# Kernel tuning notes

Measured on AMD Instinct MI355X. Metric: run time of the kernel, lower is better.

## Reference

```python
import jax, jax.numpy as jnp
import numpy as np

P_DROP = 0.2
NEG_SLOPE = 0.2


def setup_inputs() -> dict:
    key = jax.random.key(0)
    ks = jax.random.split(key, 12)
    N, E = 50000, 800000
    IN, H1, H2, OUT = 256, 256, 128, 64
    x = jax.random.normal(ks[0], (N, IN), dtype=jnp.float32)
    adj_rows = jax.random.randint(ks[1], (E,), 0, N, dtype=jnp.int32)
    adj_cols = jax.random.randint(ks[2], (E,), 0, N, dtype=jnp.int32)
    adj_vals = jax.random.uniform(ks[3], (E,), dtype=jnp.float32)
    W1 = jax.random.normal(ks[4], (H1, IN), dtype=jnp.float32) * (1.0 / np.sqrt(IN))
    b1 = jax.random.normal(ks[5], (H1,), dtype=jnp.float32) * 0.01
    W2 = jax.random.normal(ks[6], (H2, H1), dtype=jnp.float32) * (1.0 / np.sqrt(H1))
    b2 = jax.random.normal(ks[7], (H2,), dtype=jnp.float32) * 0.01
    W3 = jax.random.normal(ks[8], (OUT, H2), dtype=jnp.float32) * (1.0 / np.sqrt(H2))
    b3 = jax.random.normal(ks[9], (OUT,), dtype=jnp.float32) * 0.01
    mask1 = jax.random.bernoulli(ks[10], 1.0 - P_DROP, (N, H1))
    mask2 = jax.random.bernoulli(ks[11], 1.0 - P_DROP, (N, H2))
    return {"x": x, "adj_rows": adj_rows, "adj_cols": adj_cols, "adj_vals": adj_vals,
            "W1": W1, "b1": b1, "W2": W2, "b2": b2, "W3": W3, "b3": b3,
            "mask1": mask1, "mask2": mask2}


def _spmm(rows, cols, vals, h, n_nodes):
    # sparse adjacency matmul: out[r] = sum_e vals[e] * h[cols[e]] for rows[e]==r
    msgs = vals[:, None] * h[cols]  # [E, d] irregular gather
    return jax.ops.segment_sum(msgs, rows, num_segments=n_nodes)


def _gcn_layer(x, W, b, rows, cols, vals, n_nodes):
    h = x @ W.T + b  # nn.Linear
    return _spmm(rows, cols, vals, h, n_nodes)


def reference(x, adj_rows, adj_cols, adj_vals, W1, b1, W2, b2, W3, b3, mask1, mask2):
    N = x.shape[0]
    keep = 1.0 / (1.0 - P_DROP)
    h = _gcn_layer(x, W1, b1, adj_rows, adj_cols, adj_vals, N)
    h = jnp.where(h >= 0, h, NEG_SLOPE * h)
    h = jnp.where(mask1, h * keep, 0.0)
    h = _gcn_layer(h, W2, b2, adj_rows, adj_cols, adj_vals, N)
    h = jnp.where(h >= 0, h, NEG_SLOPE * h)
    h = jnp.where(mask2, h * keep, 0.0)
    z = _gcn_layer(h, W3, b3, adj_rows, adj_cols, adj_vals, N)
    return z
```

## Files before the change

### kernel.cpp

```cpp
#include <hip/hip_runtime.h>


typedef unsigned short ushort_t;
typedef __attribute__((ext_vector_type(8))) short bf16x8;
typedef __attribute__((ext_vector_type(4))) float f32x4;
typedef __attribute__((ext_vector_type(2))) unsigned int u32x2;
typedef __attribute__((ext_vector_type(4))) unsigned int u32x4;

__device__ __forceinline__ float bf2f(ushort_t u) {
  return __uint_as_float(((unsigned int)u) << 16);
}
__device__ __forceinline__ ushort_t f2bf(float f) {
  unsigned int u = __float_as_uint(f);
  return (ushort_t)((u + 0x7FFFu + ((u >> 16) & 1u)) >> 16);
}
__device__ __forceinline__ float read_f(const void* p, int fm, size_t i) {
  return fm ? bf2f(((const ushort_t*)p)[i]) : ((const float*)p)[i];
}

__device__ __forceinline__ size_t frag_off(int m, int k, int K) {
  return (size_t)(m >> 4) * 16 * K + ((size_t)(k >> 5) << 9) +
         (((k >> 3) & 3) << 7) + ((m & 15) << 3) + (k & 7);
}

__device__ __forceinline__ bool mask_keep(const void* mask, int mm, size_t o) {
  switch (mm) {
    case 1:  return ((const int*)mask)[o] != 0;
    case 2:  return ((const unsigned int*)mask)[o] != 0u;
    case 3:  return ((const ushort_t*)mask)[o] != 0;
    default: return ((const unsigned char*)mask)[o] != 0;
  }
}

__global__ void prep_kernel(const void* __restrict__ x,
                            const void* __restrict__ m1,
                            const void* __restrict__ m2,
                            int* __restrict__ modes,
                            int* __restrict__ zero_region, int zn) {
  if (blockIdx.x == 0) {
    __shared__ int bfok;
    if (threadIdx.x == 0) bfok = 1;
    __syncthreads();
    for (int i = threadIdx.x; i < 8192; i += blockDim.x) {
      ushort_t h = ((const ushort_t*)x)[i];
      int e = (h >> 7) & 0xFF;
      if (!(h == 0 || (e >= 95 && e <= 133))) atomicAnd(&bfok, 0);
    }
    __syncthreads();
    if (threadIdx.x == 0) modes[0] = bfok;
  } else if (blockIdx.x <= 2) {
    const void* p = (blockIdx.x == 1) ? m1 : m2;
    __shared__ int ok[4];
    if (threadIdx.x < 4) ok[threadIdx.x] = 1;
    __syncthreads();
    for (int i = threadIdx.x; i < 4096; i += blockDim.x) {
      unsigned int w = ((const unsigned int*)p)[i];
      if (!(w == 0u || w == 1u)) atomicAnd(&ok[0], 0);
      if (!(w == 0u || w == 0x3F800000u)) atomicAnd(&ok[1], 0);
      unsigned int h16 = w >> 16, l16 = w & 0xFFFFu;
      if (!((h16 == 0u || h16 == 0x3F80u) && (l16 == 0u || l16 == 0x3F80u)))
        atomicAnd(&ok[2], 0);
      if (((w | (w >> 8) | (w >> 16) | (w >> 24)) & 0xFEu) != 0u) atomicAnd(&ok[3], 0);
    }
    __syncthreads();
    if (threadIdx.x == 0)
      modes[blockIdx.x] = ok[0] ? 1 : (ok[1] ? 2 : (ok[2] ? 3 : 0));
  } else {
    int i = (blockIdx.x - 3) * blockDim.x + threadIdx.x;
    int stride = (gridDim.x - 3) * blockDim.x;
    for (; i < zn; i += stride) zero_region[i] = 0;
  }
}

__global__ void hist_kernel(const int* __restrict__ rows, int* __restrict__ cnt, int E) {
  int i = blockIdx.x * blockDim.x + threadIdx.x;
  int stride = gridDim.x * blockDim.x;
  for (; i < E; i += stride) atomicAdd(&cnt[rows[i]], 1);
}

__global__ void scan_part_kernel(const int* __restrict__ cnt, int* __restrict__ part, int n) {
  __shared__ int s[256];
  int i = blockIdx.x * 256 + threadIdx.x;
  s[threadIdx.x] = (i < n) ? cnt[i] : 0;
  __syncthreads();
  for (int off = 128; off > 0; off >>= 1) {
    if (threadIdx.x < off) s[threadIdx.x] += s[threadIdx.x + off];
    __syncthreads();
  }
  if (threadIdx.x == 0) part[blockIdx.x] = s[0];
}

__global__ __launch_bounds__(1024) void scan_top_kernel(int* __restrict__ part, int P) {
  __shared__ int s[1024];
  int t = threadIdx.x;
  int v = (t < P) ? part[t] : 0;
  s[t] = v;
  __syncthreads();
  for (int off = 1; off < 1024; off <<= 1) {
    int x = s[t];
    int y = (t >= off) ? s[t - off] : 0;
    __syncthreads();
    s[t] = x + y;
    __syncthreads();
  }
  if (t < P) part[t] = s[t] - v;
}

__global__ void scan_apply_kernel(const int* __restrict__ cnt, const int* __restrict__ part,
                                  int* __restrict__ row_start, int n) {
  __shared__ int s[256];
  int base = part[blockIdx.x];
  int i = blockIdx.x * 256 + threadIdx.x;
  int v = (i < n) ? cnt[i] : 0;
  s[threadIdx.x] = v;
  __syncthreads();
  for (int off = 1; off < 256; off <<= 1) {
    int x = s[threadIdx.x];
    int y = (threadIdx.x >= off) ? s[threadIdx.x - off] : 0;
    __syncthreads();
    s[threadIdx.x] = x + y;
    __syncthreads();
  }
  if (i < n) row_start[i] = base + s[threadIdx.x] - v;
  if (i == n - 1) row_start[n] = base + s[threadIdx.x];
}

__global__ void scatter_convert_kernel(
    const int* __restrict__ rows, const int* __restrict__ cols,
    const void* __restrict__ vals, const int* __restrict__ fm_p,
    const int* __restrict__ row_start, int* __restrict__ fill,
    int2* __restrict__ ecv, int E,
    const void* __restrict__ W1, const void* __restrict__ W2, const void* __restrict__ W3,
    const void* __restrict__ b1, const void* __restrict__ b2, const void* __restrict__ b3,
    const void* __restrict__ x,
    ushort_t* __restrict__ whi, ushort_t* __restrict__ wlo,
    float* __restrict__ biasf, ushort_t* __restrict__ xbf,
    int n1, int n2, int n3, int h1, int h2, int h3, int K1, int K2, int K3, int nx) {
  int fm = *fm_p;
  if (blockIdx.x < 1024) {
    int i = blockIdx.x * blockDim.x + threadIdx.x;
    int stride = 1024 * blockDim.x;
    for (; i < E; i += stride) {
      int r = rows[i];
      int pos = atomicAdd(&fill[r], 1);
      int idx = row_start[r] + pos;
      ecv[idx] = make_int2(cols[i], __float_as_int(read_f(vals, fm, i)));
    }
  } else {
    int wtot = n1 + n2 + n3;
    int btot = h1 + h2 + h3;
    int nx4 = nx / 4;
    int total = wtot + btot + nx4;
    int i = (blockIdx.x - 1024) * blockDim.x + threadIdx.x;
    int stride = (gridDim.x - 1024) * blockDim.x;
    for (; i < total; i += stride) {
      if (i < wtot) {
        const void* src; int j, K; size_t base;
        if (i < n1) { src = W1; j = i; K = K1; base = 0; }
        else if (i < n1 + n2) { src = W2; j = i - n1; K = K2; base = n1; }
        else { src = W3; j = i - n1 - n2; K = K3; base = (size_t)n1 + n2; }
        int n = j / K, k = j - n * K;
        float v = read_f(src, fm, j);
        ushort_t h = f2bf(v);
        size_t o = base + frag_off(n, k, K);
        whi[o] = h;
        wlo[o] = f2bf(v - bf2f(h));
      } else if (i < wtot + btot) {
        int k = i - wtot;
        const void* src; int j;
        if (k < h1) { src = b1; j = k; }
        else if (k < h1 + h2) { src = b2; j = k - h1; }
        else { src = b3; j = k - h1 - h2; }
        biasf[k] = read_f(src, fm, j);
      } else {
        int k4 = i - wtot - btot;
        int m = k4 / (K1 / 4);
        int k0 = (k4 - m * (K1 / 4)) * 4;
        ushort_t p0, p1, p2, p3;
        if (fm == 0) {
          f32x4 v = ((const f32x4*)x)[k4];
          p0 = f2bf(v[0]); p1 = f2bf(v[1]); p2 = f2bf(v[2]); p3 = f2bf(v[3]);
        } else {
          const ushort_t* xb = (const ushort_t*)x + (size_t)k4 * 4;
          p0 = xb[0]; p1 = xb[1]; p2 = xb[2]; p3 = xb[3];
        }
        size_t o = frag_off(m, k0, K1);
        *(u32x2*)(xbf + o) = (u32x2){
            (unsigned int)p0 | ((unsigned int)p1 << 16),
            (unsigned int)p2 | ((unsigned int)p3 << 16)};
      }
    }
  }
}

template<int KC>
__global__ __launch_bounds__(256) void gemm_breg_kernel(
    const ushort_t* __restrict__ A,
    const ushort_t* __restrict__ Whi, const ushort_t* __restrict__ Wlo,
    const float* __restrict__ bias, ushort_t* __restrict__ g, int ldg,
    int M, int nct) {
  const int K = KC * 32;
  int wave = threadIdx.x >> 6, lane = threadIdx.x & 63;
  int gw = blockIdx.x * 4 + wave;
  int NW = gridDim.x * 4;
  int mr = lane & 15, quad = lane >> 4;
  int ct = gw % nct;
  int nrt = (M + 15) >> 4;
  int ntasks = nct * nrt;
  if (gw >= ntasks) return;

  bf16x8 wh[KC], wl[KC];
  {
    const ushort_t* wp = Whi + (size_t)ct * 16 * K + lane * 8;
    const ushort_t* wq = Wlo + (size_t)ct * 16 * K + lane * 8;
#pragma unroll
    for (int kc = 0; kc < KC; ++kc) {
      wh[kc] = *(const bf16x8*)(wp + kc * 512);
      wl[kc] = *(const bf16x8*)(wq + kc * 512);
    }
  }
  int col = ct * 16 + mr;
  float bv = bias[col];

  int task = gw;
  bf16x8 af[KC];
  {
    const ushort_t* ap = A + (size_t)(task / nct) * 16 * K + lane * 8;
#pragma unroll
    for (int kc = 0; kc < KC; ++kc) af[kc] = *(const bf16x8*)(ap + kc * 512);
  }

#pragma unroll 1
  for (;;) {
    int next = task + NW;
    bool has_next = next < ntasks;
    bf16x8 afn[KC];
    if (has_next) {
      const ushort_t* ap = A + (size_t)(next / nct) * 16 * K + lane * 8;
#pragma unroll
      for (int kc = 0; kc < KC; ++kc) afn[kc] = *(const bf16x8*)(ap + kc * 512);
    }

    f32x4 acc[4];
#pragma unroll
    for (int t = 0; t < 4; ++t) acc[t] = (f32x4){0.f, 0.f, 0.f, 0.f};
#pragma unroll
    for (int kc = 0; kc < KC; ++kc) {
      acc[(2 * kc) & 3] = __builtin_amdgcn_mfma_f32_16x16x32_bf16(af[kc], wh[kc], acc[(2 * kc) & 3], 0, 0, 0);
      acc[(2 * kc + 1) & 3] = __builtin_amdgcn_mfma_f32_16x16x32_bf16(af[kc], wl[kc], acc[(2 * kc + 1) & 3], 0, 0, 0);
    }
    int m0 = (task / nct) * 16;
#pragma unroll
    for (int r = 0; r < 4; ++r) {
      int row = m0 + quad * 4 + r;
      float s = ((acc[0][r] + acc[1][r]) + (acc[2][r] + acc[3][r])) + bv;
      if (row < M) g[(size_t)row * ldg + col] = f2bf(s);
    }
    if (!has_next) break;
#pragma unroll
    for (int kc = 0; kc < KC; ++kc) af[kc] = afn[kc];
    task = next;
  }
}

template<int MODE, int VEC>
__global__ __launch_bounds__(256) void spmm8_kernel(
    const int* __restrict__ row_start, const int2* __restrict__ ecv,
    const ushort_t* __restrict__ G, int D,
    const void* __restrict__ mask, const int* __restrict__ mmode_p,
    void* __restrict__ outp, int N) {
  __shared__ ushort_t stage[1024];
  int wave = threadIdx.x >> 6, lane = threadIdx.x & 63;
  int r = blockIdx.x * 4 + wave;
  bool active = r < N;
  float a[VEC];
#pragma unroll
  for (int q = 0; q < VEC; ++q) a[q] = 0.f;
  int f0 = lane * VEC;

  if (active) {
    int e  = __builtin_amdgcn_readfirstlane(row_start[r]);
    int e1 = __builtin_amdgcn_readfirstlane(row_start[r + 1]);
    for (; e + 8 <= e1; e += 8) {
      int2 cv[8];
#pragma unroll
      for (int j = 0; j < 8; ++j) cv[j] = ecv[e + j];
      if (VEC == 4) {
        u32x2 gg[8];
#pragma unroll
        for (int j = 0; j < 8; ++j)
          gg[j] = *(const u32x2*)(G + (size_t)cv[j].x * D + f0);
#pragma unroll
        for (int j = 0; j < 8; ++j) {
          float v = __int_as_float(cv[j].y);
          a[0] += v * bf2f((ushort_t)gg[j][0]);
          a[1] += v * bf2f((ushort_t)(gg[j][0] >> 16));
          a[2] += v * bf2f((ushort_t)gg[j][1]);
          a[3] += v * bf2f((ushort_t)(gg[j][1] >> 16));
        }
      } else if (VEC == 2) {
        unsigned int gg[8];
#pragma unroll
        for (int j = 0; j < 8; ++j)
          gg[j] = *(const unsigned int*)(G + (size_t)cv[j].x * D + f0);
#pragma unroll
        for (int j = 0; j < 8; ++j) {
          float v = __int_as_float(cv[j].y);
          a[0] += v * bf2f((ushort_t)gg[j]);
          a[1] += v * bf2f((ushort_t)(gg[j] >> 16));
        }
      } else {
        ushort_t h[8];
#pragma unroll
        for (int j = 0; j < 8; ++j) h[j] = G[(size_t)cv[j].x * D + f0];
#pragma unroll
        for (int j = 0; j < 8; ++j) a[0] += __int_as_float(cv[j].y) * bf2f(h[j]);
      }
    }
    if (e < e1) {
      int idx[8]; float v[8];
#pragma unroll
      for (int j = 0; j < 8; ++j) {
        int ee = e + j;
        bool ok = ee < e1;
        int2 cv = ecv[ok ? ee : e1 - 1];
        idx[j] = cv.x;
        v[j] = ok ? __int_as_float(cv.y) : 0.f;
      }
      if (VEC == 4) {
        u32x2 gg[8];
#pragma unroll
        for (int j = 0; j < 8; ++j)
          gg[j] = *(const u32x2*)(G + (size_t)idx[j] * D + f0);
#pragma unroll
        for (int j = 0; j < 8; ++j) {
          a[0] += v[j] * bf2f((ushort_t)gg[j][0]);
          a[1] += v[j] * bf2f((ushort_t)(gg[j][0] >> 16));
          a[2] += v[j] * bf2f((ushort_t)gg[j][1]);
          a[3] += v[j] * bf2f((ushort_t)(gg[j][1] >> 16));
        }
      } else if (VEC == 2) {
        unsigned int gg[8];
#pragma unroll
        for (int j = 0; j < 8; ++j)
          gg[j] = *(const unsigned int*)(G + (size_t)idx[j] * D + f0);
#pragma unroll
        for (int j = 0; j < 8; ++j) {
          a[0] += v[j] * bf2f((ushort_t)gg[j]);
          a[1] += v[j] * bf2f((ushort_t)(gg[j] >> 16));
        }
      } else {
        ushort_t h[8];
#pragma unroll
        for (int j = 0; j < 8; ++j) h[j] = G[(size_t)idx[j] * D + f0];
#pragma unroll
        for (int j = 0; j < 8; ++j) a[0] += v[j] * bf2f(h[j]);
      }
    }
  }

  if (MODE == 1) {
    if (active) {
      size_t om = (size_t)r * D + f0;
      int mm = *mmode_p;
      bool keep[VEC];
      if (mm == 1 || mm == 2) {
        if (VEC == 4) {
          u32x4 mv = *(const u32x4*)((const unsigned int*)mask + om);
#pragma unroll
          for (int q = 0; q < VEC; ++q) keep[q] = mv[q] != 0u;
        } else if (VEC == 2) {
          u32x2 mv = *(const u32x2*)((const unsigned int*)mask + om);
#pragma unroll
          for (int q = 0; q < VEC; ++q) keep[q] = mv[q] != 0u;
        } else {
          keep[0] = ((const unsigned int*)mask)[om] != 0u;
        }
      } else {
#pragma unroll
        for (int q = 0; q < VEC; ++q) keep[q] = mask_keep(mask, mm, om + q);
      }
#pragma unroll
      for (int q = 0; q < VEC; ++q) {
        float t = a[q];
        t = (t >= 0.f) ? t : 0.2f * t;
        t = keep[q] ? t * 1.25f : 0.f;
        stage[wave * D + f0 + q] = f2bf(t);
      }
    }
    __syncthreads();
    if (threadIdx.x < D) {
      int g = threadIdx.x >> 3, s = threadIdx.x & 7;
      int kc = g >> 2, quad = g & 3;
      int sr = s >> 1;
      int r0 = blockIdx.x * 4;
      if (r0 + sr < N) {
        int kk = kc * 32 + quad * 8 + (s & 1) * 4;
        size_t dst = (size_t)(r0 >> 4) * 16 * D + ((size_t)kc << 9) +
                     (quad << 7) + ((r0 & 15) << 3) + s * 4;
        *(u32x2*)((ushort_t*)outp + dst) = *(const u32x2*)(stage + sr * D + kk);
      }
    }
  } else {
    if (active) {
      size_t o = (size_t)r * D + f0;
#pragma unroll
      for (int q = 0; q < VEC; ++q) ((float*)outp)[o + q] = a[q];
    }
  }
}

extern "C" void kernel_launch(void* const* d_in, const int* in_sizes, int n_in,
                              void* d_out, int out_size, void* d_ws, size_t ws_size,
                              hipStream_t stream) {
  const void* x     = d_in[0];
  const int*  rows  = (const int*)d_in[1];
  const int*  cols  = (const int*)d_in[2];
  const void* vals  = d_in[3];
  const void* W1    = d_in[4];
  const void* b1    = d_in[5];
  const void* W2    = d_in[6];
  const void* b2    = d_in[7];
  const void* W3    = d_in[8];
  const void* b3    = d_in[9];
  const void* mask1 = d_in[10];
  const void* mask2 = d_in[11];

  const int H1  = in_sizes[5];
  const int H2  = in_sizes[7];
  const int OUT = in_sizes[9];
  const int IN  = in_sizes[4] / H1;
  const int N   = in_sizes[0] / IN;
  const int E   = in_sizes[1];
  const int W1n = in_sizes[4], W2n = in_sizes[6], W3n = in_sizes[8];
  const int Np  = ((N + 15) / 16) * 16;

  char* ws = (char*)d_ws;
  size_t off = 0;
  auto alloc = [&](size_t bytes) -> void* {
    void* p = ws + off;
    off = (off + bytes + 255) & ~(size_t)255;
    return p;
  };
  int*      modes     = (int*)alloc(4 * 4);
  int*      row_start = (int*)alloc((size_t)(N + 1) * 4);
  int*      cnt       = (int*)alloc((size_t)N * 8);
  int*      part      = (int*)alloc(1024 * 4);
  int2*     ecv       = (int2*)alloc((size_t)E * 8);
  ushort_t* whi       = (ushort_t*)alloc((size_t)(W1n + W2n + W3n) * 2);
  ushort_t* wlo       = (ushort_t*)alloc((size_t)(W1n + W2n + W3n) * 2);
  float*    biasf     = (float*)alloc((size_t)(H1 + H2 + OUT) * 4);
  ushort_t* bufA      = (ushort_t*)alloc((size_t)Np * H1 * 2);
  ushort_t* bufB      = (ushort_t*)alloc((size_t)Np * H1 * 2);
  ushort_t* bufC      = (ushort_t*)alloc((size_t)Np * H1 * 2);

  int* fmode = modes;
  int* mm1   = modes + 1;
  int* mm2   = modes + 2;
  int* fill  = cnt + N;
  ushort_t* w1hi = whi,             *w1lo = wlo;
  ushort_t* w2hi = whi + W1n,       *w2lo = wlo + W1n;
  ushort_t* w3hi = whi + W1n + W2n, *w3lo = wlo + W1n + W2n;

  prep_kernel<<<259, 256, 0, stream>>>(x, mask1, mask2, modes, cnt, 2 * N);

  const int P = (N + 255) / 256;
  hist_kernel<<<1024, 256, 0, stream>>>(rows, cnt, E);
  scan_part_kernel<<<P, 256, 0, stream>>>(cnt, part, N);
  scan_top_kernel<<<1, 1024, 0, stream>>>(part, P);
  scan_apply_kernel<<<P, 256, 0, stream>>>(cnt, part, row_start, N);

  scatter_convert_kernel<<<3072, 256, 0, stream>>>(
      rows, cols, vals, fmode, row_start, fill, ecv, E,
      W1, W2, W3, b1, b2, b3, x, whi, wlo, biasf, bufA,
      W1n, W2n, W3n, H1, H2, OUT, IN, H1, H2, N * IN);

  const int GEMM_BLOCKS = 1024;
  int spmm_grid = (N + 3) / 4;

  gemm_breg_kernel<8><<<GEMM_BLOCKS, 256, 0, stream>>>(
      bufA, w1hi, w1lo, biasf, bufB, H1, N, H1 / 16);
  spmm8_kernel<1, 4><<<spmm_grid, 256, 0, stream>>>(
      row_start, ecv, bufB, H1, mask1, mm1, bufC, N);
  gemm_breg_kernel<8><<<GEMM_BLOCKS, 256, 0, stream>>>(
      bufC, w2hi, w2lo, biasf + H1, bufB, H2, N, H2 / 16);
  spmm8_kernel<1, 2><<<spmm_grid, 256, 0, stream>>>(
      row_start, ecv, bufB, H2, mask2, mm2, bufA, N);
  gemm_breg_kernel<4><<<GEMM_BLOCKS, 256, 0, stream>>>(
      bufA, w3hi, w3lo, biasf + H1 + H2, bufB, OUT, N, OUT / 16);
  spmm8_kernel<0, 1><<<spmm_grid, 256, 0, stream>>>(
      row_start, ecv, bufB, OUT, nullptr, fmode, d_out, N);
}
```

Baseline: 438.3 us.

## Partition edge scatter by row range and read bf16 x directly in GEMM

The edge scatter now splits blocks into eight row-range partitions. Each block scans a stripe of edges and only handles edges whose destination row falls in its partition, which is meant to improve locality of the atomic fill counters and ecv writes. The cost is that every partition reads the full rows array, so rows is read eight times. When the input is bf16 (fm==1), the x re-layout pass is skipped and the first GEMM loads A fragments straight from row-major x. The mask reading also gains vectorized paths for 16-bit and byte masks.

Measured after the change: 432.1 us. Within noise of the previous version (-1.4%).

```diff
diff --git a/kernel.cpp b/kernel.cpp
--- a/kernel.cpp
+++ b/kernel.cpp
@@ -135,13 +135,20 @@
     const void* __restrict__ x,
     ushort_t* __restrict__ whi, ushort_t* __restrict__ wlo,
     float* __restrict__ biasf, ushort_t* __restrict__ xbf,
-    int n1, int n2, int n3, int h1, int h2, int h3, int K1, int K2, int K3, int nx) {
+    int n1, int n2, int n3, int h1, int h2, int h3, int K1, int K2, int K3,
+    int nx, int Nrows) {
   int fm = *fm_p;
   if (blockIdx.x < 1024) {
-    int i = blockIdx.x * blockDim.x + threadIdx.x;
-    int stride = 1024 * blockDim.x;
+    int part = blockIdx.x & 7;
+    int stripe = blockIdx.x >> 3;
+    float pscale = 8.0f / (float)Nrows;
+    int i = stripe * blockDim.x + threadIdx.x;
+    int stride = 128 * blockDim.x;
     for (; i < E; i += stride) {
       int r = rows[i];
+      int p = (int)((float)r * pscale);
+      p = (p > 7) ? 7 : p;
+      if (p != part) continue;
       int pos = atomicAdd(&fill[r], 1);
       int idx = row_start[r] + pos;
       ecv[idx] = make_int2(cols[i], __float_as_int(read_f(vals, fm, i)));
@@ -149,7 +156,7 @@
   } else {
     int wtot = n1 + n2 + n3;
     int btot = h1 + h2 + h3;
-    int nx4 = nx / 4;
+    int nx4 = (fm == 1) ? 0 : nx / 4;
     int total = wtot + btot + nx4;
     int i = (blockIdx.x - 1024) * blockDim.x + threadIdx.x;
     int stride = (gridDim.x - 1024) * blockDim.x;
@@ -176,14 +183,8 @@
         int k4 = i - wtot - btot;
         int m = k4 / (K1 / 4);
         int k0 = (k4 - m * (K1 / 4)) * 4;
-        ushort_t p0, p1, p2, p3;
-        if (fm == 0) {
-          f32x4 v = ((const f32x4*)x)[k4];
-          p0 = f2bf(v[0]); p1 = f2bf(v[1]); p2 = f2bf(v[2]); p3 = f2bf(v[3]);
-        } else {
-          const ushort_t* xb = (const ushort_t*)x + (size_t)k4 * 4;
-          p0 = xb[0]; p1 = xb[1]; p2 = xb[2]; p3 = xb[3];
-        }
+        f32x4 v = ((const f32x4*)x)[k4];
+        ushort_t p0 = f2bf(v[0]), p1 = f2bf(v[1]), p2 = f2bf(v[2]), p3 = f2bf(v[3]);
         size_t o = frag_off(m, k0, K1);
         *(u32x2*)(xbf + o) = (u32x2){
             (unsigned int)p0 | ((unsigned int)p1 << 16),
@@ -194,8 +195,28 @@
 }
 
 template<int KC>
+__device__ __forceinline__ void load_afrag(const ushort_t* __restrict__ A,
+                                           const ushort_t* __restrict__ Xrow,
+                                           bool rowA, int mtile, int K,
+                                           int lane, int mr, int quad, int M,
+                                           bf16x8* dst) {
+  if (rowA) {
+    int rr = mtile * 16 + mr;
+    if (rr >= M) rr = M - 1;
+    const ushort_t* ap = Xrow + (size_t)rr * K + quad * 8;
+#pragma unroll
+    for (int kc = 0; kc < KC; ++kc) dst[kc] = *(const bf16x8*)(ap + kc * 32);
+  } else {
+    const ushort_t* ap = A + (size_t)mtile * 16 * K + lane * 8;
+#pragma unroll
+    for (int kc = 0; kc < KC; ++kc) dst[kc] = *(const bf16x8*)(ap + kc * 512);
+  }
+}
+
+template<int KC>
 __global__ __launch_bounds__(256) void gemm_breg_kernel(
     const ushort_t* __restrict__ A,
+    const ushort_t* __restrict__ Xrow, const int* __restrict__ fm_p,
     const ushort_t* __restrict__ Whi, const ushort_t* __restrict__ Wlo,
     const float* __restrict__ bias, ushort_t* __restrict__ g, int ldg,
     int M, int nct) {
@@ -209,6 +230,8 @@
   int ntasks = nct * nrt;
   if (gw >= ntasks) return;
 
+  bool rowA = (Xrow != nullptr) && (*fm_p != 0);
+
   bf16x8 wh[KC], wl[KC];
   {
     const ushort_t* wp = Whi + (size_t)ct * 16 * K + lane * 8;
@@ -224,22 +247,15 @@
 
   int task = gw;
   bf16x8 af[KC];
-  {
-    const ushort_t* ap = A + (size_t)(task / nct) * 16 * K + lane * 8;
-#pragma unroll
-    for (int kc = 0; kc < KC; ++kc) af[kc] = *(const bf16x8*)(ap + kc * 512);
-  }
+  load_afrag<KC>(A, Xrow, rowA, task / nct, K, lane, mr, quad, M, af);
 
 #pragma unroll 1
   for (;;) {
     int next = task + NW;
     bool has_next = next < ntasks;
     bf16x8 afn[KC];
-    if (has_next) {
-      const ushort_t* ap = A + (size_t)(next / nct) * 16 * K + lane * 8;
-#pragma unroll
-      for (int kc = 0; kc < KC; ++kc) afn[kc] = *(const bf16x8*)(ap + kc * 512);
-    }
+    if (has_next)
+      load_afrag<KC>(A, Xrow, rowA, next / nct, K, lane, mr, quad, M, afn);
 
     f32x4 acc[4];
 #pragma unroll
@@ -376,9 +392,28 @@
         } else {
           keep[0] = ((const unsigned int*)mask)[om] != 0u;
         }
+      } else if (mm == 3) {
+        if (VEC == 4) {
+          u32x2 mv = *(const u32x2*)((const ushort_t*)mask + om);
+          keep[0] = (mv[0] & 0xFFFFu) != 0u; keep[1] = (mv[0] >> 16) != 0u;
+          keep[2] = (mv[1] & 0xFFFFu) != 0u; keep[3] = (mv[1] >> 16) != 0u;
+        } else if (VEC == 2) {
+          unsigned int mv = *(const unsigned int*)((const ushort_t*)mask + om);
+          keep[0] = (mv & 0xFFFFu) != 0u; keep[1] = (mv >> 16) != 0u;
+        } else {
+          keep[0] = ((const ushort_t*)mask)[om] != 0;
+        }
       } else {
-#pragma unroll
-        for (int q = 0; q < VEC; ++q) keep[q] = mask_keep(mask, mm, om + q);
+        if (VEC == 4) {
+          unsigned int mv = *(const unsigned int*)((const unsigned char*)mask + om);
+          keep[0] = (mv & 0xFFu) != 0u;        keep[1] = ((mv >> 8) & 0xFFu) != 0u;
+          keep[2] = ((mv >> 16) & 0xFFu) != 0u; keep[3] = (mv >> 24) != 0u;
+        } else if (VEC == 2) {
+          unsigned int mv = *(const unsigned short*)((const unsigned char*)mask + om);
+          keep[0] = (mv & 0xFFu) != 0u; keep[1] = ((mv >> 8) & 0xFFu) != 0u;
+        } else {
+          keep[0] = ((const unsigned char*)mask)[om] != 0;
+        }
       }
 #pragma unroll
       for (int q = 0; q < VEC; ++q) {
@@ -473,21 +508,21 @@
   scatter_convert_kernel<<<3072, 256, 0, stream>>>(
       rows, cols, vals, fmode, row_start, fill, ecv, E,
       W1, W2, W3, b1, b2, b3, x, whi, wlo, biasf, bufA,
-      W1n, W2n, W3n, H1, H2, OUT, IN, H1, H2, N * IN);
+      W1n, W2n, W3n, H1, H2, OUT, IN, H1, H2, N * IN, N);
 
   const int GEMM_BLOCKS = 1024;
   int spmm_grid = (N + 3) / 4;
 
   gemm_breg_kernel<8><<<GEMM_BLOCKS, 256, 0, stream>>>(
-      bufA, w1hi, w1lo, biasf, bufB, H1, N, H1 / 16);
+      bufA, (const ushort_t*)x, fmode, w1hi, w1lo, biasf, bufB, H1, N, H1 / 16);
   spmm8_kernel<1, 4><<<spmm_grid, 256, 0, stream>>>(
       row_start, ecv, bufB, H1, mask1, mm1, bufC, N);
   gemm_breg_kernel<8><<<GEMM_BLOCKS, 256, 0, stream>>>(
-      bufC, w2hi, w2lo, biasf + H1, bufB, H2, N, H2 / 16);
+      bufC, nullptr, fmode, w2hi, w2lo, biasf + H1, bufB, H2, N, H2 / 16);
   spmm8_kernel<1, 2><<<spmm_grid, 256, 0, stream>>>(
       row_start, ecv, bufB, H2, mask2, mm2, bufA, N);
   gemm_breg_kernel<4><<<GEMM_BLOCKS, 256, 0, stream>>>(
-      bufA, w3hi, w3lo, biasf + H1 + H2, bufB, OUT, N, OUT / 16);
+      bufA, nullptr, fmode, w3hi, w3lo, biasf + H1 + H2, bufB, OUT, N, OUT / 16);
   spmm8_kernel<0, 1><<<spmm_grid, 256, 0, stream>>>(
       row_start, ecv, bufB, OUT, nullptr, fmode, d_out, N);
 }
```
